# Optimization experiments

Hardware: AMD Instinct MI355X
Metric: run time of the kernel (lower is better)

Reference implementation:

```python
import jax, jax.numpy as jnp
import numpy as np

N, E, G = 30000, 480000, 64
IN, MID, HEADS, OUT = 256, (64, 64, 128), 8, 13


def _tconv(x, src, dst, ea, qw, qb, kw, kb, vw, vb, ew, sw, sb, heads, n):
    # PyG TransformerConv (concat=True, root_weight=True, beta=False), eval mode
    d = qw.shape[1] // heads
    q = (x @ qw + qb)[dst].reshape(-1, heads, d)   # [E,H,d] query at target
    k = (x @ kw + kb)[src].reshape(-1, heads, d)   # [E,H,d] key at source
    v = (x @ vw + vb)[src].reshape(-1, heads, d)   # [E,H,d] value at source
    e = (ea @ ew).reshape(-1, heads, d)            # [E,H,d] edge embedding (no bias)
    k = k + e
    a = (q * k).sum(-1) / jnp.sqrt(jnp.asarray(d, x.dtype))   # [E,H]
    amax = jax.ops.segment_max(a, dst, num_segments=n)        # segment softmax over in-edges
    ex = jnp.exp(a - amax[dst])
    den = jax.ops.segment_sum(ex, dst, num_segments=n)
    alpha = ex / den[dst]
    out = jax.ops.segment_sum((v + e) * alpha[..., None], dst, num_segments=n)
    out = out.reshape(n, heads * d)
    return out + x @ sw + sb                        # root/skip connection


def _mk(key, shape):
    return jax.random.normal(key, shape, dtype=jnp.float32) * 0.05


def setup_inputs() -> dict:
    key = jax.random.key(0)
    ks = iter(jax.random.split(key, 40))
    inp = {
        "x": jax.random.normal(next(ks), (N, IN), dtype=jnp.float32),
        "edge_index": jax.random.randint(next(ks), (2, E), 0, N, dtype=jnp.int64),
        "edge_attr": jax.random.normal(next(ks), (E, 1), dtype=jnp.float32),
        "batch": jnp.sort(jax.random.randint(next(ks), (N,), 0, G, dtype=jnp.int64)),
    }
    # conv1: in=256 -> heads=8, d=64 (out 512)
    o1 = HEADS * MID[0]
    inp.update(q1w=_mk(next(ks), (IN, o1)), q1b=_mk(next(ks), (o1,)),
               k1w=_mk(next(ks), (IN, o1)), k1b=_mk(next(ks), (o1,)),
               v1w=_mk(next(ks), (IN, o1)), v1b=_mk(next(ks), (o1,)),
               e1w=_mk(next(ks), (1, o1)),
               s1w=_mk(next(ks), (IN, o1)), s1b=_mk(next(ks), (o1,)))
    # conv2: in=512 -> heads=4, d=64 (out 256)
    h2, i2 = HEADS // 2, o1
    o2 = h2 * MID[1]
    inp.update(q2w=_mk(next(ks), (i2, o2)), q2b=_mk(next(ks), (o2,)),
               k2w=_mk(next(ks), (i2, o2)), k2b=_mk(next(ks), (o2,)),
               v2w=_mk(next(ks), (i2, o2)), v2b=_mk(next(ks), (o2,)),
               e2w=_mk(next(ks), (1, o2)),
               s2w=_mk(next(ks), (i2, o2)), s2b=_mk(next(ks), (o2,)))
    # conv3: in=256 -> heads=1, d=128
    i3, o3 = o2, MID[2]
    inp.update(q3w=_mk(next(ks), (i3, o3)), q3b=_mk(next(ks), (o3,)),
               k3w=_mk(next(ks), (i3, o3)), k3b=_mk(next(ks), (o3,)),
               v3w=_mk(next(ks), (i3, o3)), v3b=_mk(next(ks), (o3,)),
               e3w=_mk(next(ks), (1, o3)),
               s3w=_mk(next(ks), (i3, o3)), s3b=_mk(next(ks), (o3,)))
    inp.update(lw=_mk(next(ks), (MID[2], OUT)), lb=_mk(next(ks), (OUT,)))
    return inp


def reference(x, edge_index, edge_attr, batch,
              q1w, q1b, k1w, k1b, v1w, v1b, e1w, s1w, s1b,
              q2w, q2b, k2w, k2b, v2w, v2b, e2w, s2w, s2b,
              q3w, q3b, k3w, k3b, v3w, v3b, e3w, s3w, s3b,
              lw, lb):
    src, dst = edge_index[0], edge_index[1]
    h = _tconv(x, src, dst, edge_attr, q1w, q1b, k1w, k1b, v1w, v1b, e1w, s1w, s1b, HEADS, N)
    h = jax.nn.relu(h)
    h = _tconv(h, src, dst, edge_attr, q2w, q2b, k2w, k2b, v2w, v2b, e2w, s2w, s2b, HEADS // 2, N)
    h = jax.nn.relu(h)
    h = _tconv(h, src, dst, edge_attr, q3w, q3b, k3w, k3b, v3w, v3b, e3w, s3w, s3b, 1, N)
    # global mean pool over graphs
    s = jax.ops.segment_sum(h, batch, num_segments=G)
    cnt = jax.ops.segment_sum(jnp.ones((N,), h.dtype), batch, num_segments=G)
    pooled = s / jnp.maximum(cnt, 1.0)[:, None]
    return pooled @ lw + lb
```

## Files before the change

kernel.cpp:

```cpp
#include <hip/hip_runtime.h>
#include <hip/hip_bf16.h>
#include <cstdint>

#define NN 30000
#define EE 480000
#define GG 64

typedef __attribute__((ext_vector_type(8))) short bf16x8;
typedef __attribute__((ext_vector_type(4))) float float4v;
typedef __attribute__((ext_vector_type(2))) float f32x2;
typedef __attribute__((ext_vector_type(4))) unsigned short ushort4v;

static __device__ inline unsigned short f2bf(float f) {
    unsigned u = __float_as_uint(f);
    unsigned r = (u + 0x7fff + ((u >> 16) & 1)) >> 16;
    return (unsigned short)r;
}
static __device__ inline float bf2f(unsigned short u) {
    return __uint_as_float(((unsigned)u) << 16);
}

__global__ void count_deg_k(const int* __restrict__ ei, int* __restrict__ deg) {
    int e = blockIdx.x * 256 + threadIdx.x;
    if (e < EE) atomicAdd(&deg[ei[EE + e]], 1);
}

__global__ __launch_bounds__(1024) void scan_excl_k(const int* __restrict__ deg,
                                                    int* __restrict__ basep) {
    constexpr int CH = (NN + 1024) / 1024 + 1;
    __shared__ int buf[1024];
    int t = threadIdx.x;
    int b0 = t * CH;
    int loc[CH];
    int s = 0;
#pragma unroll
    for (int i = 0; i < CH; i++) {
        int idx = b0 + i;
        int v = (idx < NN) ? deg[idx] : 0;
        loc[i] = s;
        s += v;
    }
    buf[t] = s;
    __syncthreads();
    for (int off = 1; off < 1024; off <<= 1) {
        int tv = (t >= off) ? buf[t - off] : 0;
        __syncthreads();
        buf[t] += tv;
        __syncthreads();
    }
    int base = (t > 0) ? buf[t - 1] : 0;
#pragma unroll
    for (int i = 0; i < CH; i++) {
        int idx = b0 + i;
        if (idx <= NN) basep[idx] = base + loc[i];
    }
}

__global__ void fill_csr_k(const int* __restrict__ ei, const float* __restrict__ ea,
                           const int* __restrict__ basep, int* __restrict__ cnt,
                           int* __restrict__ csrc, float* __restrict__ cea) {
    int e = blockIdx.x * 256 + threadIdx.x;
    if (e < EE) {
        int d = ei[EE + e];
        int pos = basep[d] + atomicAdd(&cnt[d], 1);
        csrc[pos] = ei[e];
        cea[pos] = ea[e];
    }
}

__global__ void gbound_k(const int* __restrict__ batch, int* __restrict__ gstart) {
    int i = blockIdx.x * 256 + threadIdx.x;
    if (i >= NN) return;
    int cur = batch[i];
    if (i == 0) {
        for (int g = 0; g <= cur; ++g) gstart[g] = 0;
    } else {
        int prev = batch[i - 1];
        for (int g = prev + 1; g <= cur; ++g) gstart[g] = i;
    }
    if (i == NN - 1) {
        for (int g = cur + 1; g <= GG; ++g) gstart[g] = NN;
    }
}

struct PrepDesc { const float* src; void* dst; int rows; int cols; int blk0; int mode; };
#define NDESC 25
struct PrepArgs { PrepDesc d[NDESC]; };

__global__ __launch_bounds__(256) void prep_k(PrepArgs args) {
    int b = blockIdx.x;
    PrepDesc dd = args.d[0];
#pragma unroll
    for (int i = 1; i < NDESC; i++)
        if (b >= args.d[i].blk0) dd = args.d[i];
    int rel = b - dd.blk0;
    int total = dd.rows * dd.cols;
    int base = rel * 1024 + threadIdx.x;
    if (dd.mode == 0) {
        unsigned short* dst = (unsigned short*)dd.dst;
        for (int j = 0; j < 4; j++) {
            int i = base + j * 256;
            if (i < total) dst[i] = f2bf(dd.src[i]);
        }
    } else if (dd.mode == 1) {
        unsigned short* dst = (unsigned short*)dd.dst;
        for (int j = 0; j < 4; j++) {
            int i = base + j * 256;
            if (i < total) {
                int n = i / dd.rows, k = i - n * dd.rows;
                dst[i] = f2bf(dd.src[(size_t)k * dd.cols + n]);
            }
        }
    } else {
        float* dst = (float*)dd.dst;
        for (int j = 0; j < 4; j++) {
            int i = base + j * 256;
            if (i < total) dst[i] = dd.src[i];
        }
    }
}

__global__ __launch_bounds__(256) void gemm_bf16_k(
    const unsigned short* __restrict__ A, const unsigned short* __restrict__ Wt,
    const float* __restrict__ bias, unsigned short* __restrict__ C,
    unsigned char* __restrict__ KV8,
    int M, int K, int N) {
    __shared__ unsigned short As[3][4096];
    __shared__ unsigned short Bs[3][4096];
    int tid = threadIdx.x;
    int lane = tid & 63, wid = tid >> 6;
    int wm = wid >> 1, wn = wid & 1;

    int gx = gridDim.x;
    int T = gx * gridDim.y;
    int lid = blockIdx.y * gx + blockIdx.x;
    int qq = T >> 3, rr = T & 7;
    int xcd = lid & 7, pos = lid >> 3;
    int tile = ((xcd < rr) ? xcd * (qq + 1) : rr * (qq + 1) + (xcd - rr) * qq) + pos;
    int by = tile / gx, bx = tile - by * gx;
    int row0 = by * 128, n0 = bx * 128;

    float4v acc[4][4];
#pragma unroll
    for (int i = 0; i < 4; i++)
#pragma unroll
        for (int j = 0; j < 4; j++) acc[i][j] = (float4v)0.f;

    auto stage = [&](int buf, int t) {
        int k0 = t << 5;
#pragma unroll
        for (int i = 0; i < 2; ++i) {
            int chunkbase = i * 256 + wid * 64;
            int chunk = chunkbase + lane;
            int r = chunk & 127, kc = chunk >> 7;
            int rowA = row0 + r; if (rowA >= M) rowA = M - 1;
            const unsigned short* ga = A + (size_t)rowA * K + (k0 + kc * 8);
            __builtin_amdgcn_global_load_lds(
                (const __attribute__((address_space(1))) void*)ga,
                (__attribute__((address_space(3))) void*)(As[buf] + (size_t)chunkbase * 8),
                16, 0, 0);
            const unsigned short* gb = Wt + (size_t)(n0 + r) * K + (k0 + kc * 8);
            __builtin_amdgcn_global_load_lds(
                (const __attribute__((address_space(1))) void*)gb,
                (__attribute__((address_space(3))) void*)(Bs[buf] + (size_t)chunkbase * 8),
                16, 0, 0);
        }
    };

    int NT = K >> 5;
    stage(0, 0);
    stage(1, 1);

    for (int t = 0; t < NT; ++t) {
        int b = t % 3;
        if (t + 1 < NT) asm volatile("s_waitcnt vmcnt(4)" ::: "memory");
        else            asm volatile("s_waitcnt vmcnt(0)" ::: "memory");
        __syncthreads();
        if (t + 2 < NT) stage((t + 2) % 3, t + 2);

        bf16x8 af[4], bfr[4];
#pragma unroll
        for (int mi = 0; mi < 4; mi++)
            af[mi] = *(const bf16x8*)(As[b] + ((lane >> 4) * 128 + wm * 64 + mi * 16 + (lane & 15)) * 8);
#pragma unroll
        for (int ni = 0; ni < 4; ni++)
            bfr[ni] = *(const bf16x8*)(Bs[b] + ((lane >> 4) * 128 + wn * 64 + ni * 16 + (lane & 15)) * 8);
#pragma unroll
        for (int mi = 0; mi < 4; mi++)
#pragma unroll
            for (int ni = 0; ni < 4; ni++)
                acc[mi][ni] = __builtin_amdgcn_mfma_f32_16x16x32_bf16(
                    bfr[ni], af[mi], acc[mi][ni], 0, 0, 0);
    }

    int kvlo = N >> 2, kvhi = 3 * (N >> 2);
    float4v bias4[4];
#pragma unroll
    for (int ni = 0; ni < 4; ni++)
        bias4[ni] = *(const float4v*)&bias[n0 + wn * 64 + ni * 16 + (lane >> 4) * 4];
#pragma unroll
    for (int mi = 0; mi < 4; mi++) {
        int row = row0 + wm * 64 + mi * 16 + (lane & 15);
        if (row < M) {
#pragma unroll
            for (int ni = 0; ni < 4; ni++) {
                int colb = n0 + wn * 64 + ni * 16 + (lane >> 4) * 4;
                float v0 = acc[mi][ni][0] + bias4[ni][0];
                float v1 = acc[mi][ni][1] + bias4[ni][1];
                float v2 = acc[mi][ni][2] + bias4[ni][2];
                float v3 = acc[mi][ni][3] + bias4[ni][3];
                ushort4v pk;
                pk[0] = f2bf(v0); pk[1] = f2bf(v1); pk[2] = f2bf(v2); pk[3] = f2bf(v3);
                *(ushort4v*)(C + (size_t)row * N + colb) = pk;
                if (colb >= kvlo && colb < kvhi) {
                    unsigned q = 0;
                    q = __builtin_amdgcn_cvt_pk_fp8_f32(v0, v1, q, false);
                    q = __builtin_amdgcn_cvt_pk_fp8_f32(v2, v3, q, true);
                    *(unsigned*)(KV8 + (size_t)row * (N >> 1) + (colb - kvlo)) = q;
                }
            }
        }
    }
}

template <int VEC> struct RawVec;
template <> struct RawVec<2> { using T = unsigned; };
template <> struct RawVec<4> { using T = uint2; };
template <> struct RawVec<8> { using T = uint4; };

template <int VEC> struct Raw8;
template <> struct Raw8<2> { using T = unsigned short; };
template <> struct Raw8<4> { using T = unsigned; };
template <> struct Raw8<8> { using T = uint2; };

static __device__ inline void unpackr(unsigned v, float (&r)[2]) {
    r[0] = __uint_as_float(v << 16); r[1] = __uint_as_float(v & 0xffff0000u);
}
static __device__ inline void unpackr(uint2 v, float (&r)[4]) {
    r[0] = __uint_as_float(v.x << 16); r[1] = __uint_as_float(v.x & 0xffff0000u);
    r[2] = __uint_as_float(v.y << 16); r[3] = __uint_as_float(v.y & 0xffff0000u);
}
static __device__ inline void unpackr(uint4 v, float (&r)[8]) {
    r[0] = __uint_as_float(v.x << 16); r[1] = __uint_as_float(v.x & 0xffff0000u);
    r[2] = __uint_as_float(v.y << 16); r[3] = __uint_as_float(v.y & 0xffff0000u);
    r[4] = __uint_as_float(v.z << 16); r[5] = __uint_as_float(v.z & 0xffff0000u);
    r[6] = __uint_as_float(v.w << 16); r[7] = __uint_as_float(v.w & 0xffff0000u);
}

static __device__ inline void unpackf8(unsigned short v, float (&r)[2]) {
    f32x2 a = __builtin_amdgcn_cvt_pk_f32_fp8((unsigned)v, false);
    r[0] = a[0]; r[1] = a[1];
}
static __device__ inline void unpackf8(unsigned v, float (&r)[4]) {
    f32x2 a0 = __builtin_amdgcn_cvt_pk_f32_fp8(v, false);
    f32x2 a1 = __builtin_amdgcn_cvt_pk_f32_fp8(v, true);
    r[0] = a0[0]; r[1] = a0[1]; r[2] = a1[0]; r[3] = a1[1];
}
static __device__ inline void unpackf8(uint2 v, float (&r)[8]) {
    f32x2 a0 = __builtin_amdgcn_cvt_pk_f32_fp8(v.x, false);
    f32x2 a1 = __builtin_amdgcn_cvt_pk_f32_fp8(v.x, true);
    f32x2 a2 = __builtin_amdgcn_cvt_pk_f32_fp8(v.y, false);
    f32x2 a3 = __builtin_amdgcn_cvt_pk_f32_fp8(v.y, true);
    r[0] = a0[0]; r[1] = a0[1]; r[2] = a1[0]; r[3] = a1[1];
    r[4] = a2[0]; r[5] = a2[1]; r[6] = a3[0]; r[7] = a3[1];
}

template <int VEC>
__device__ inline void loadbf(const unsigned short* __restrict__ p, float (&r)[VEC]) {
    typename RawVec<VEC>::T v = *(const typename RawVec<VEC>::T*)p;
    unpackr(v, r);
}
template <int VEC>
__device__ inline void loadf32(const float* __restrict__ p, float (&r)[VEC]) {
    if constexpr (VEC == 2) {
        float2 t = *reinterpret_cast<const float2*>(p);
        r[0] = t.x; r[1] = t.y;
    } else {
#pragma unroll
        for (int i = 0; i < VEC; i += 4) {
            float4 t = *reinterpret_cast<const float4*>(p + i);
            r[i] = t.x; r[i + 1] = t.y; r[i + 2] = t.z; r[i + 3] = t.w;
        }
    }
}
template <int VEC>
__device__ inline void storebf(unsigned short* __restrict__ p, const float (&r)[VEC]) {
    unsigned w[VEC / 2];
#pragma unroll
    for (int i = 0; i < VEC / 2; i++)
        w[i] = (unsigned)f2bf(r[2 * i]) | ((unsigned)f2bf(r[2 * i + 1]) << 16);
    if constexpr (VEC == 2) *(unsigned*)p = w[0];
    else if constexpr (VEC == 4) *(uint2*)p = make_uint2(w[0], w[1]);
    else *(uint4*)p = make_uint4(w[0], w[1], w[2], w[3]);
}

template <int H, int D, bool RELU>
__global__ __launch_bounds__(256) void aggregate_k(
    const unsigned short* __restrict__ QKVS, int SR,
    const unsigned char* __restrict__ KV8,
    const float* __restrict__ ew,
    const int* __restrict__ rowptr, const int* __restrict__ csrc,
    const float* __restrict__ cea, unsigned short* __restrict__ Hout) {
    constexpr int F = H * D;
    constexpr int VEC = F / 64;
    constexpr int L = 64 / H;
    using RawT = typename Raw8<VEC>::T;
    int lane = threadIdx.x & 63;
    int node = blockIdx.x * 4 + (threadIdx.x >> 6);
    if (node >= NN) return;

    const unsigned short* qrow = QKVS + (size_t)node * SR;
    float q[VEC], ewv[VEC], acc[VEC];
    loadbf<VEC>(qrow + lane * VEC, q);
    loadf32<VEC>(ew + lane * VEC, ewv);
#pragma unroll
    for (int i = 0; i < VEC; i++) acc[i] = 0.f;

    float den = 0.f;
    const float isd = rsqrtf((float)D);
    int beg = rowptr[node], end = rowptr[node + 1];

    for (int cb = beg; cb < end; cb += 64) {
        int cnt = min(end - cb, 64);
        int gi = cb + lane;
        int sidx = (gi < end) ? csrc[gi] : 0;
        float sea = (gi < end) ? cea[gi] : 0.f;

        RawT k0r, k1r, k2r, k3r, v0r, v1r, v2r, v3r;
        float e0 = 0.f, e1 = 0.f, e2 = 0.f, e3 = 0.f;
        auto fetch = [&](int t, RawT& kr, RawT& vr, float& ea) {
            int s = __shfl(sidx, t, 64);
            ea = __shfl(sea, t, 64);
            const unsigned char* b = KV8 + (size_t)s * (2 * F) + lane * VEC;
            kr = *(const RawT*)b;
            vr = *(const RawT*)(b + F);
        };
        auto process = [&](RawT kr, RawT vr, float ea) {
            float kv[VEC], vv[VEC], t[VEC];
            unpackf8(kr, kv);
            unpackf8(vr, vv);
            float p = 0.f;
#pragma unroll
            for (int i = 0; i < VEC; i++) { t[i] = ea * ewv[i]; p += q[i] * (kv[i] + t[i]); }
#pragma unroll
            for (int off = 1; off < L; off <<= 1) p += __shfl_xor(p, off, 64);
            float w = __expf(fminf(p * isd, 30.f));
            den += w;
#pragma unroll
            for (int i = 0; i < VEC; i++) acc[i] += w * (vv[i] + t[i]);
        };

        if (cnt > 0) fetch(0, k0r, v0r, e0);
        if (cnt > 1) fetch(1, k1r, v1r, e1);
        if (cnt > 2) fetch(2, k2r, v2r, e2);
        if (cnt > 3) fetch(3, k3r, v3r, e3);

        for (int t = 0; t < cnt; t += 4) {
            process(k0r, v0r, e0);
            if (t + 4 < cnt) fetch(t + 4, k0r, v0r, e0);
            if (t + 1 < cnt) {
                process(k1r, v1r, e1);
                if (t + 5 < cnt) fetch(t + 5, k1r, v1r, e1);
            }
            if (t + 2 < cnt) {
                process(k2r, v2r, e2);
                if (t + 6 < cnt) fetch(t + 6, k2r, v2r, e2);
            }
            if (t + 3 < cnt) {
                process(k3r, v3r, e3);
                if (t + 7 < cnt) fetch(t + 7, k3r, v3r, e3);
            }
        }
    }

    float rden = (den > 0.f) ? 1.f / den : 0.f;
    float sv[VEC];
    loadbf<VEC>(qrow + 3 * F + lane * VEC, sv);
    float o[VEC];
#pragma unroll
    for (int i = 0; i < VEC; i++) {
        float v = acc[i] * rden + sv[i];
        o[i] = RELU ? fmaxf(v, 0.f) : v;
    }
    storebf<VEC>(Hout + (size_t)node * F + lane * VEC, o);
}

__global__ __launch_bounds__(256) void pool_head_k(
    const unsigned short* __restrict__ h3, const int* __restrict__ gstart,
    const float* __restrict__ lw, const float* __restrict__ lb,
    float* __restrict__ out) {
    __shared__ float part[256];
    __shared__ float pooled[128];
    int g = blockIdx.x;
    int beg = gstart[g], end = gstart[g + 1];
    int d = threadIdx.x & 127, half = threadIdx.x >> 7;
    float s = 0.f;
    for (int node = beg + half; node < end; node += 2)
        s += bf2f(h3[(size_t)node * 128 + d]);
    part[threadIdx.x] = s;
    __syncthreads();
    if (threadIdx.x < 128) {
        float cnt = fmaxf((float)(end - beg), 1.0f);
        pooled[threadIdx.x] = (part[threadIdx.x] + part[threadIdx.x + 128]) / cnt;
    }
    __syncthreads();
    if (threadIdx.x < 13) {
        float acc = lb[threadIdx.x];
        for (int dd = 0; dd < 128; ++dd)
            acc += pooled[dd] * lw[dd * 13 + threadIdx.x];
        out[g * 13 + threadIdx.x] = acc;
    }
}

__global__ void ws_fail_k(float* __restrict__ out, int n) {
    int i = blockIdx.x * 256 + threadIdx.x;
    if (i < n) out[i] = -12345.0f;
}

extern "C" void kernel_launch(void* const* d_in, const int* in_sizes, int n_in,
                              void* d_out, int out_size, void* d_ws, size_t ws_size,
                              hipStream_t stream) {
    const float* x   = (const float*)d_in[0];
    const int*   ei  = (const int*)d_in[1];
    const float* ea  = (const float*)d_in[2];
    const int*   bat = (const int*)d_in[3];
    const float* W1[4] = {(const float*)d_in[4], (const float*)d_in[6], (const float*)d_in[8], (const float*)d_in[11]};
    const float* B1[4] = {(const float*)d_in[5], (const float*)d_in[7], (const float*)d_in[9], (const float*)d_in[12]};
    const float* e1w = (const float*)d_in[10];
    const float* W2[4] = {(const float*)d_in[13], (const float*)d_in[15], (const float*)d_in[17], (const float*)d_in[20]};
    const float* B2[4] = {(const float*)d_in[14], (const float*)d_in[16], (const float*)d_in[18], (const float*)d_in[21]};
    const float* e2w = (const float*)d_in[19];
    const float* W3[4] = {(const float*)d_in[22], (const float*)d_in[24], (const float*)d_in[26], (const float*)d_in[29]};
    const float* B3[4] = {(const float*)d_in[23], (const float*)d_in[25], (const float*)d_in[27], (const float*)d_in[30]};
    const float* e3w = (const float*)d_in[28];
    const float* lw  = (const float*)d_in[31];
    const float* lb  = (const float*)d_in[32];

    char* wsb = (char*)d_ws;
    size_t off = 0;
    auto alloc_b = [&](size_t bytes) {
        void* p = wsb + off;
        off += (bytes + 255) & ~(size_t)255;
        return p;
    };
    unsigned short* xb   = (unsigned short*)alloc_b((size_t)NN * 256 * 2);
    unsigned short* Wc1  = (unsigned short*)alloc_b((size_t)2048 * 256 * 2);
    float*          bc1  = (float*)alloc_b(2048 * 4);
    unsigned short* Wc2  = (unsigned short*)alloc_b((size_t)1024 * 512 * 2);
    float*          bc2  = (float*)alloc_b(1024 * 4);
    unsigned short* Wc3  = (unsigned short*)alloc_b((size_t)512 * 256 * 2);
    float*          bc3  = (float*)alloc_b(512 * 4);
    unsigned short* QKVS = (unsigned short*)alloc_b((size_t)NN * 2048 * 2);
    unsigned char*  KV8  = (unsigned char*)alloc_b((size_t)NN * 1024);
    unsigned short* H1   = (unsigned short*)alloc_b((size_t)NN * 512 * 2);
    unsigned short* H2   = (unsigned short*)alloc_b((size_t)NN * 256 * 2);
    unsigned short* H3   = (unsigned short*)alloc_b((size_t)NN * 128 * 2);
    int*   basep  = (int*)alloc_b((NN + 1) * 4);
    int*   csrc   = (int*)alloc_b((size_t)EE * 4);
    float* cea    = (float*)alloc_b((size_t)EE * 4);
    int*   gstart = (int*)alloc_b((GG + 1) * 4);
    size_t zstart = off;
    int*   deg    = (int*)alloc_b(NN * 4);
    int*   cnt    = (int*)alloc_b(NN * 4);
    size_t zbytes = off - zstart;

    if (ws_size < off) {
        ws_fail_k<<<(out_size + 255) / 256, 256, 0, stream>>>((float*)d_out, out_size);
        return;
    }

    hipMemsetAsync(wsb + zstart, 0, zbytes, stream);

    PrepArgs pa;
    int blk = 0, di = 0;
    auto add = [&](const float* src, void* dst, int rows, int cols, int mode) {
        pa.d[di].src = src; pa.d[di].dst = dst;
        pa.d[di].rows = rows; pa.d[di].cols = cols;
        pa.d[di].mode = mode; pa.d[di].blk0 = blk;
        blk += (rows * cols + 1023) / 1024;
        di++;
    };
    add(x, xb, NN * 256, 1, 0);
    for (int s = 0; s < 4; s++) add(W1[s], Wc1 + (size_t)s * 512 * 256, 256, 512, 1);
    for (int s = 0; s < 4; s++) add(B1[s], bc1 + s * 512, 512, 1, 2);
    for (int s = 0; s < 4; s++) add(W2[s], Wc2 + (size_t)s * 256 * 512, 512, 256, 1);
    for (int s = 0; s < 4; s++) add(B2[s], bc2 + s * 256, 256, 1, 2);
    for (int s = 0; s < 4; s++) add(W3[s], Wc3 + (size_t)s * 128 * 256, 256, 128, 1);
    for (int s = 0; s < 4; s++) add(B3[s], bc3 + s * 128, 128, 1, 2);
    prep_k<<<blk, 256, 0, stream>>>(pa);

    int eblocks = (EE + 255) / 256;
    count_deg_k<<<eblocks, 256, 0, stream>>>(ei, deg);
    scan_excl_k<<<1, 1024, 0, stream>>>(deg, basep);
    fill_csr_k<<<eblocks, 256, 0, stream>>>(ei, ea, basep, cnt, csrc, cea);
    gbound_k<<<(NN + 255) / 256, 256, 0, stream>>>(bat, gstart);

    int mblocks = (NN + 127) / 128;
    gemm_bf16_k<<<dim3(2048 / 128, mblocks), 256, 0, stream>>>(xb, Wc1, bc1, QKVS, KV8, NN, 256, 2048);
    aggregate_k<8, 64, true><<<NN / 4, 256, 0, stream>>>(QKVS, 2048, KV8, e1w, basep, csrc, cea, H1);
    gemm_bf16_k<<<dim3(1024 / 128, mblocks), 256, 0, stream>>>(H1, Wc2, bc2, QKVS, KV8, NN, 512, 1024);
    aggregate_k<4, 64, true><<<NN / 4, 256, 0, stream>>>(QKVS, 1024, KV8, e2w, basep, csrc, cea, H2);
    gemm_bf16_k<<<dim3(512 / 128, mblocks), 256, 0, stream>>>(H2, Wc3, bc3, QKVS, KV8, NN, 256, 512);
    aggregate_k<1, 128, false><<<NN / 4, 256, 0, stream>>>(QKVS, 512, KV8, e3w, basep, csrc, cea, H3);

    pool_head_k<<<GG, 256, 0, stream>>>(H3, gstart, lw, lb, (float*)d_out);
}
```

Baseline: 728.8 us.

## Double-buffer GEMM mainloop and stage epilogue through LDS for coalesced stores

Changes the bf16 GEMM mainloop from triple-buffered prefetch-two to double-buffered prefetch-one with a full wait and barrier each iteration, and reuses the shared memory as a per-wave staging tile in the epilogue. Output tiles are written to LDS and then stored as 16-byte row-contiguous vectors to C and the fp8 KV buffer, replacing scattered 8-byte and 4-byte stores. The intent is better store coalescing. The cost is less load/compute overlap in the mainloop, and the fp8 values are now quantized from the bf16-rounded values instead of from fp32.

```diff
diff --git a/kernel.cpp b/kernel.cpp
--- a/kernel.cpp
+++ b/kernel.cpp
@@ -125,8 +125,7 @@
     const float* __restrict__ bias, unsigned short* __restrict__ C,
     unsigned char* __restrict__ KV8,
     int M, int K, int N) {
-    __shared__ unsigned short As[3][4096];
-    __shared__ unsigned short Bs[3][4096];
+    __shared__ unsigned short lds[18432];
     int tid = threadIdx.x;
     int lane = tid & 63, wid = tid >> 6;
     int wm = wid >> 1, wn = wid & 1;
@@ -146,6 +145,9 @@
 #pragma unroll
         for (int j = 0; j < 4; j++) acc[i][j] = (float4v)0.f;
 
+    auto As = [&](int b) { return lds + b * 4096; };
+    auto Bs = [&](int b) { return lds + 8192 + b * 4096; };
+
     auto stage = [&](int buf, int t) {
         int k0 = t << 5;
 #pragma unroll
@@ -157,67 +159,82 @@
             const unsigned short* ga = A + (size_t)rowA * K + (k0 + kc * 8);
             __builtin_amdgcn_global_load_lds(
                 (const __attribute__((address_space(1))) void*)ga,
-                (__attribute__((address_space(3))) void*)(As[buf] + (size_t)chunkbase * 8),
+                (__attribute__((address_space(3))) void*)(As(buf) + (size_t)chunkbase * 8),
                 16, 0, 0);
             const unsigned short* gb = Wt + (size_t)(n0 + r) * K + (k0 + kc * 8);
             __builtin_amdgcn_global_load_lds(
                 (const __attribute__((address_space(1))) void*)gb,
-                (__attribute__((address_space(3))) void*)(Bs[buf] + (size_t)chunkbase * 8),
+                (__attribute__((address_space(3))) void*)(Bs(buf) + (size_t)chunkbase * 8),
                 16, 0, 0);
         }
     };
 
     int NT = K >> 5;
     stage(0, 0);
-    stage(1, 1);
+    asm volatile("s_waitcnt vmcnt(0)" ::: "memory");
+    __syncthreads();
 
     for (int t = 0; t < NT; ++t) {
-        int b = t % 3;
-        if (t + 1 < NT) asm volatile("s_waitcnt vmcnt(4)" ::: "memory");
-        else            asm volatile("s_waitcnt vmcnt(0)" ::: "memory");
-        __syncthreads();
-        if (t + 2 < NT) stage((t + 2) % 3, t + 2);
-
+        int b = t & 1;
+        if (t + 1 < NT) stage(b ^ 1, t + 1);
         bf16x8 af[4], bfr[4];
 #pragma unroll
         for (int mi = 0; mi < 4; mi++)
-            af[mi] = *(const bf16x8*)(As[b] + ((lane >> 4) * 128 + wm * 64 + mi * 16 + (lane & 15)) * 8);
+            af[mi] = *(const bf16x8*)(As(b) + ((lane >> 4) * 128 + wm * 64 + mi * 16 + (lane & 15)) * 8);
 #pragma unroll
         for (int ni = 0; ni < 4; ni++)
-            bfr[ni] = *(const bf16x8*)(Bs[b] + ((lane >> 4) * 128 + wn * 64 + ni * 16 + (lane & 15)) * 8);
+            bfr[ni] = *(const bf16x8*)(Bs(b) + ((lane >> 4) * 128 + wn * 64 + ni * 16 + (lane & 15)) * 8);
 #pragma unroll
         for (int mi = 0; mi < 4; mi++)
 #pragma unroll
             for (int ni = 0; ni < 4; ni++)
                 acc[mi][ni] = __builtin_amdgcn_mfma_f32_16x16x32_bf16(
                     bfr[ni], af[mi], acc[mi][ni], 0, 0, 0);
-    }
-
-    int kvlo = N >> 2, kvhi = 3 * (N >> 2);
+        asm volatile("s_waitcnt vmcnt(0)" ::: "memory");
+        __syncthreads();
+    }
+
+    unsigned short* stg = lds + wid * 4608;
     float4v bias4[4];
 #pragma unroll
     for (int ni = 0; ni < 4; ni++)
         bias4[ni] = *(const float4v*)&bias[n0 + wn * 64 + ni * 16 + (lane >> 4) * 4];
 #pragma unroll
     for (int mi = 0; mi < 4; mi++) {
-        int row = row0 + wm * 64 + mi * 16 + (lane & 15);
+#pragma unroll
+        for (int ni = 0; ni < 4; ni++) {
+            ushort4v pk;
+#pragma unroll
+            for (int r = 0; r < 4; r++) pk[r] = f2bf(acc[mi][ni][r] + bias4[ni][r]);
+            *(ushort4v*)(stg + (mi * 16 + (lane & 15)) * 72 + ni * 16 + (lane >> 4) * 4) = pk;
+        }
+    }
+    int rbase = row0 + wm * 64;
+    int cbase = n0 + wn * 64;
+#pragma unroll
+    for (int it = 0; it < 8; ++it) {
+        int r = it * 8 + (lane >> 3);
+        int row = rbase + r;
         if (row < M) {
-#pragma unroll
-            for (int ni = 0; ni < 4; ni++) {
-                int colb = n0 + wn * 64 + ni * 16 + (lane >> 4) * 4;
-                float v0 = acc[mi][ni][0] + bias4[ni][0];
-                float v1 = acc[mi][ni][1] + bias4[ni][1];
-                float v2 = acc[mi][ni][2] + bias4[ni][2];
-                float v3 = acc[mi][ni][3] + bias4[ni][3];
-                ushort4v pk;
-                pk[0] = f2bf(v0); pk[1] = f2bf(v1); pk[2] = f2bf(v2); pk[3] = f2bf(v3);
-                *(ushort4v*)(C + (size_t)row * N + colb) = pk;
-                if (colb >= kvlo && colb < kvhi) {
-                    unsigned q = 0;
-                    q = __builtin_amdgcn_cvt_pk_fp8_f32(v0, v1, q, false);
-                    q = __builtin_amdgcn_cvt_pk_fp8_f32(v2, v3, q, true);
-                    *(unsigned*)(KV8 + (size_t)row * (N >> 1) + (colb - kvlo)) = q;
-                }
+            uint4 v = *(const uint4*)(stg + r * 72 + (lane & 7) * 8);
+            *(uint4*)(C + (size_t)row * N + cbase + (lane & 7) * 8) = v;
+        }
+    }
+    int kvlo = N >> 2, kvhi = 3 * (N >> 2);
+    if (cbase >= kvlo && cbase < kvhi) {
+#pragma unroll
+        for (int it = 0; it < 8; ++it) {
+            int r = it * 8 + (lane >> 3);
+            int row = rbase + r;
+            if (row < M) {
+                const unsigned short* p = stg + r * 72 + (lane & 7) * 8;
+                unsigned lo = 0, hi = 0;
+                lo = __builtin_amdgcn_cvt_pk_fp8_f32(bf2f(p[0]), bf2f(p[1]), lo, false);
+                lo = __builtin_amdgcn_cvt_pk_fp8_f32(bf2f(p[2]), bf2f(p[3]), lo, true);
+                hi = __builtin_amdgcn_cvt_pk_fp8_f32(bf2f(p[4]), bf2f(p[5]), hi, false);
+                hi = __builtin_amdgcn_cvt_pk_fp8_f32(bf2f(p[6]), bf2f(p[7]), hi, true);
+                *(uint2*)(KV8 + (size_t)row * (N >> 1) + (cbase - kvlo) + (lane & 7) * 8) =
+                    make_uint2(lo, hi);
             }
         }
     }
```

Measured after the change: 672.2 us. 7.8% less time.
